# Kernel tuning notes

Measured on AMD Instinct MI355X. Metric: run time of the kernel, lower is better.

The kernel has to match this reference:

```python
import jax, jax.numpy as jnp
import numpy as np

B, K, T, V, H = 32, 5, 20, 9488, 1024


def setup_inputs() -> dict:
    key = jax.random.key(0)
    k0, k1, k2, k3, k4 = jax.random.split(key, 5)
    logprobs = jax.nn.log_softmax(jax.random.normal(k0, (B * K, V), jnp.float32), -1)
    beam_seq = jax.random.randint(k1, (B, K, T), 0, V)
    beam_seq_logprobs = jax.random.normal(k2, (B, K, T, V), jnp.float32)
    beam_logprobs_sum = jax.random.normal(k3, (B, K), jnp.float32)
    state = jax.random.normal(k4, (2, B * K, H), jnp.float32)
    return {"logprobs": logprobs, "beam_seq": beam_seq,
            "beam_seq_logprobs": beam_seq_logprobs,
            "beam_logprobs_sum": beam_logprobs_sum, "state": state,
            "beam_size": K, "t": T}


def reference(logprobs, beam_seq, beam_seq_logprobs, beam_logprobs_sum, state, beam_size, t):
    # One beam_step of CaptionModel.beam_search.
    batch = beam_logprobs_sum.shape[0]
    vocab = logprobs.shape[-1]
    lp = logprobs.reshape(batch, -1, vocab)                  # [B, K, V]
    cand = beam_logprobs_sum[:, :, None] + lp                # [B, K, V]
    flat = cand.reshape(batch, -1)                           # [B, K*V]
    # torch.sort(desc)[:, :beam_size] == top_k (sorted descending)
    ys, ix = jax.lax.top_k(flat, beam_size)                  # [B, K]
    beam_ix = ix // vocab                                    # source beam  [B, K]
    selected_ix = ix % vocab                                 # chosen word  [B, K]
    brange = jnp.arange(batch)[:, None]
    state_ix = (beam_ix + brange * lp.shape[1]).reshape(-1)  # [B*K]

    if t > 0:
        beam_seq = beam_seq[brange, beam_ix]                             # [B, K, t]
        beam_seq_logprobs = beam_seq_logprobs[brange, beam_ix]           # [B, K, t, V]
    beam_seq = jnp.concatenate([beam_seq, selected_ix[:, :, None].astype(beam_seq.dtype)], -1)

    beam_logprobs_sum = (jnp.take_along_axis(beam_logprobs_sum, beam_ix, 1)
                         + jnp.take_along_axis(lp.reshape(batch, -1), ix, 1))  # [B, K]

    beam_lp = lp[brange, beam_ix]                            # [B, K, V]
    beam_seq_logprobs = jnp.concatenate([beam_seq_logprobs, beam_lp[:, :, None, :]], 2)

    new_state = state[:, state_ix]                           # [layers, B*K, H]
    return beam_seq, beam_seq_logprobs, beam_logprobs_sum, new_state
```

## Files before the change

### kernel.cpp

```cpp
#include <hip/hip_runtime.h>

#define BB 32
#define KK 5
#define TT 20
#define VV 9488
#define HH 1024
#define NSPLIT 16
#define CHUNK (VV / NSPLIT)

#define OFF1 3360
#define OFF2 31883040
#define OFF3 31883200

typedef float f4 __attribute__((ext_vector_type(4)));

__device__ __forceinline__ bool better(float av, int ai, float bv, int bi) {
    return (av > bv) || (av == bv && ai < bi);
}

__device__ __forceinline__ void insert5(float tv[5], int ti[5], float val, int idx) {
#pragma unroll
    for (int j = 4; j >= 1; --j) {
        bool bj  = better(val, idx, tv[j],   ti[j]);
        bool bj1 = better(val, idx, tv[j-1], ti[j-1]);
        float nv = bj ? (bj1 ? tv[j-1] : val) : tv[j];
        int   ni = bj ? (bj1 ? ti[j-1] : idx) : ti[j];
        tv[j] = nv; ti[j] = ni;
    }
    bool b0 = better(val, idx, tv[0], ti[0]);
    ti[0] = b0 ? idx : ti[0];
    tv[0] = b0 ? val : tv[0];
}

__device__ __forceinline__ void merge_sorted5(float av[5], int ai[5],
                                              const float bv[5], const int bi[5]) {
    float ov[5]; int oi[5];
#pragma unroll
    for (int n = 0; n < 5; ++n) {
        float mv = 0.f; int mi = 0;
#pragma unroll
        for (int i = 0; i <= n; ++i) {
            const int j = n - i;
            float cv; int ci;
            if (better(av[i], ai[i], bv[j], bi[j])) { cv = av[i]; ci = ai[i]; }
            else                                    { cv = bv[j]; ci = bi[j]; }
            if (i == 0 || better(mv, mi, cv, ci)) { mv = cv; mi = ci; }
        }
        ov[n] = mv; oi[n] = mi;
    }
#pragma unroll
    for (int n = 0; n < 5; ++n) { av[n] = ov[n]; ai[n] = oi[n]; }
}

template<int MAXST>
__device__ __forceinline__ void wave_merge(float tv[5], int ti[5]) {
#pragma unroll
    for (int st = 1; st <= MAXST; st <<= 1) {
        float bv[5]; int bi[5];
#pragma unroll
        for (int j = 0; j < 5; ++j) {
            bv[j] = __shfl_xor(tv[j], st);
            bi[j] = __shfl_xor(ti[j], st);
        }
        merge_sorted5(tv, ti, bv, bi);
    }
}

__global__ __launch_bounds__(256) void topk_part_kernel(
    const float* __restrict__ logprobs,
    const float* __restrict__ sums,
    float* __restrict__ pv,
    int*   __restrict__ pi)
{
    const int b    = blockIdx.x / NSPLIT;
    const int part = blockIdx.x % NSPLIT;
    const int tid  = threadIdx.x;
    const int v0   = part * CHUNK;

    float tv[5]; int ti[5];
#pragma unroll
    for (int j = 0; j < 5; ++j) { tv[j] = -INFINITY; ti[j] = 0x7FFFFF00 + j; }

#pragma unroll
    for (int k = 0; k < KK; ++k) {
        const float s = sums[b * KK + k];
        const float* lp = logprobs + (size_t)(b * KK + k) * VV;
        for (int v = v0 + tid; v < v0 + CHUNK; v += 256)
            insert5(tv, ti, s + lp[v], k * VV + v);
    }

    wave_merge<32>(tv, ti);

    __shared__ float lv[4][5];
    __shared__ int   li[4][5];
    const int wid = tid >> 6, lane = tid & 63;
    if (lane == 0) {
#pragma unroll
        for (int j = 0; j < 5; ++j) { lv[wid][j] = tv[j]; li[wid][j] = ti[j]; }
    }
    __syncthreads();
    if (tid < 64) {
        if (tid < 4) {
#pragma unroll
            for (int j = 0; j < 5; ++j) { tv[j] = lv[tid][j]; ti[j] = li[tid][j]; }
        } else {
#pragma unroll
            for (int j = 0; j < 5; ++j) { tv[j] = -INFINITY; ti[j] = 0x7FFFFF00 + j; }
        }
        wave_merge<2>(tv, ti);
        if (tid == 0) {
#pragma unroll
            for (int j = 0; j < 5; ++j) {
                pv[(size_t)blockIdx.x * 5 + j] = tv[j];
                pi[(size_t)blockIdx.x * 5 + j] = ti[j];
            }
        }
    }
}

__global__ __launch_bounds__(64) void topk_merge_kernel(
    const float* __restrict__ pv,
    const int*   __restrict__ pi,
    int*   __restrict__ ws_beam,
    int*   __restrict__ ws_sel,
    float* __restrict__ ws_sum)
{
    const int b   = blockIdx.x;
    const int tid = threadIdx.x;

    float tv[5]; int ti[5];
    if (tid < NSPLIT) {
        const size_t base = ((size_t)b * NSPLIT + tid) * 5;
#pragma unroll
        for (int j = 0; j < 5; ++j) { tv[j] = pv[base + j]; ti[j] = pi[base + j]; }
    } else {
#pragma unroll
        for (int j = 0; j < 5; ++j) { tv[j] = -INFINITY; ti[j] = 0x7FFFFF00 + j; }
    }

    wave_merge<8>(tv, ti);

    if (tid == 0) {
#pragma unroll
        for (int j = 0; j < 5; ++j) {
            const int idx  = ti[j];
            const int beam = idx / VV;
            ws_beam[b * KK + j] = beam;
            ws_sel [b * KK + j] = idx - beam * VV;
            ws_sum [b * KK + j] = tv[j];
        }
    }
}

__global__ __launch_bounds__(256) void scatter_kernel(
    const float* __restrict__ logprobs,
    const int*   __restrict__ beam_seq_in,
    const float* __restrict__ bslp_in,
    const float* __restrict__ state_in,
    const int*   __restrict__ ws_beam,
    const int*   __restrict__ ws_sel,
    const float* __restrict__ ws_sum,
    float* __restrict__ out)
{
    const int bid = blockIdx.x;
    const int tid = threadIdx.x;
    const int NROWS = BB * KK * (TT + 1);

    if (bid < NROWS) {
        const int b   = bid / (KK * (TT + 1));
        const int rem = bid % (KK * (TT + 1));
        const int k   = rem / (TT + 1);
        const int t   = rem % (TT + 1);
        const int beam = ws_beam[b * KK + k];
        const float* src = (t < TT)
            ? bslp_in  + ((size_t)((b * KK + beam) * TT + t)) * VV
            : logprobs + (size_t)(b * KK + beam) * VV;
        const f4* s4 = (const f4*)src;
        f4* d4 = (f4*)(out + OFF1 + (size_t)bid * VV);
        for (int i = tid; i < VV / 4; i += 256) d4[i] = s4[i];
    } else if (bid < NROWS + 2 * BB * KK) {
        const int r = bid - NROWS;
        const int s = r / (BB * KK);
        const int i = r % (BB * KK);
        const int b = i / KK;
        const int beam = ws_beam[i];
        const f4* s4 = (const f4*)(state_in + ((size_t)s * (BB * KK) + b * KK + beam) * HH);
        f4* d4 = (f4*)(out + OFF3 + (size_t)r * HH);
        for (int j = tid; j < HH / 4; j += 256) d4[j] = s4[j];
    } else {
        for (int j = tid; j < NROWS; j += 256) {
            const int b   = j / (KK * (TT + 1));
            const int rem = j % (KK * (TT + 1));
            const int k   = rem / (TT + 1);
            const int t   = rem % (TT + 1);
            const int bk  = b * KK + k;
            int val;
            if (t < TT) val = beam_seq_in[(size_t)(b * KK + ws_beam[bk]) * TT + t];
            else        val = ws_sel[bk];
            out[j] = (float)val;
        }
        for (int j = tid; j < BB * KK; j += 256) out[OFF2 + j] = ws_sum[j];
    }
}

extern "C" void kernel_launch(void* const* d_in, const int* in_sizes, int n_in,
                              void* d_out, int out_size, void* d_ws, size_t ws_size,
                              hipStream_t stream) {
    const float* logprobs = (const float*)d_in[0];
    const int*   beam_seq = (const int*)  d_in[1];
    const float* bslp     = (const float*)d_in[2];
    const float* sums     = (const float*)d_in[3];
    const float* state    = (const float*)d_in[4];

    float* pv      = (float*)d_ws;
    int*   pi      = (int*)(pv + BB * NSPLIT * 5);
    int*   ws_beam = pi + BB * NSPLIT * 5;
    int*   ws_sel  = ws_beam + BB * KK;
    float* ws_sum  = (float*)(ws_sel + BB * KK);
    float* out     = (float*)d_out;

    topk_part_kernel<<<BB * NSPLIT, 256, 0, stream>>>(logprobs, sums, pv, pi);
    topk_merge_kernel<<<BB, 64, 0, stream>>>(pv, pi, ws_beam, ws_sel, ws_sum);

    const int nblocks = 3360 + 320 + 1;
    scatter_kernel<<<nblocks, 256, 0, stream>>>(logprobs, beam_seq, bslp, state,
                                                ws_beam, ws_sel, ws_sum, out);
}
```

Before: 65.41 us.

## Fuse top-k partial and merge kernels into one 1024-thread block per batch

Replaces the two-stage top-k (16 partial blocks per batch plus a merge kernel) with a single kernel using one 1024-thread block per batch that scans all beams and does the full wave and shared-memory merge. This removes one kernel launch and the workspace round trip for partial results. In exchange, only 32 blocks run the top-k phase, which lowers parallelism across the GPU. The scatter copy loop is also unrolled by two to keep more loads in flight, and the state copy uses a single load per thread.

```diff
diff --git a/kernel.cpp b/kernel.cpp
--- a/kernel.cpp
+++ b/kernel.cpp
@@ -5,8 +5,6 @@
 #define TT 20
 #define VV 9488
 #define HH 1024
-#define NSPLIT 16
-#define CHUNK (VV / NSPLIT)
 
 #define OFF1 3360
 #define OFF2 31883040
@@ -66,16 +64,15 @@
     }
 }
 
-__global__ __launch_bounds__(256) void topk_part_kernel(
+__global__ __launch_bounds__(1024) void topk_kernel(
     const float* __restrict__ logprobs,
     const float* __restrict__ sums,
-    float* __restrict__ pv,
-    int*   __restrict__ pi)
+    int*   __restrict__ ws_beam,
+    int*   __restrict__ ws_sel,
+    float* __restrict__ ws_sum)
 {
-    const int b    = blockIdx.x / NSPLIT;
-    const int part = blockIdx.x % NSPLIT;
-    const int tid  = threadIdx.x;
-    const int v0   = part * CHUNK;
+    const int b   = blockIdx.x;
+    const int tid = threadIdx.x;
 
     float tv[5]; int ti[5];
 #pragma unroll
@@ -85,14 +82,14 @@
     for (int k = 0; k < KK; ++k) {
         const float s = sums[b * KK + k];
         const float* lp = logprobs + (size_t)(b * KK + k) * VV;
-        for (int v = v0 + tid; v < v0 + CHUNK; v += 256)
+        for (int v = tid; v < VV; v += 1024)
             insert5(tv, ti, s + lp[v], k * VV + v);
     }
 
     wave_merge<32>(tv, ti);
 
-    __shared__ float lv[4][5];
-    __shared__ int   li[4][5];
+    __shared__ float lv[16][5];
+    __shared__ int   li[16][5];
     const int wid = tid >> 6, lane = tid & 63;
     if (lane == 0) {
 #pragma unroll
@@ -100,54 +97,23 @@
     }
     __syncthreads();
     if (tid < 64) {
-        if (tid < 4) {
+        if (tid < 16) {
 #pragma unroll
             for (int j = 0; j < 5; ++j) { tv[j] = lv[tid][j]; ti[j] = li[tid][j]; }
         } else {
 #pragma unroll
             for (int j = 0; j < 5; ++j) { tv[j] = -INFINITY; ti[j] = 0x7FFFFF00 + j; }
         }
-        wave_merge<2>(tv, ti);
+        wave_merge<8>(tv, ti);
         if (tid == 0) {
 #pragma unroll
             for (int j = 0; j < 5; ++j) {
-                pv[(size_t)blockIdx.x * 5 + j] = tv[j];
-                pi[(size_t)blockIdx.x * 5 + j] = ti[j];
+                const int idx  = ti[j];
+                const int beam = idx / VV;
+                ws_beam[b * KK + j] = beam;
+                ws_sel [b * KK + j] = idx - beam * VV;
+                ws_sum [b * KK + j] = tv[j];
             }
-        }
-    }
-}
-
-__global__ __launch_bounds__(64) void topk_merge_kernel(
-    const float* __restrict__ pv,
-    const int*   __restrict__ pi,
-    int*   __restrict__ ws_beam,
-    int*   __restrict__ ws_sel,
-    float* __restrict__ ws_sum)
-{
-    const int b   = blockIdx.x;
-    const int tid = threadIdx.x;
-
-    float tv[5]; int ti[5];
-    if (tid < NSPLIT) {
-        const size_t base = ((size_t)b * NSPLIT + tid) * 5;
-#pragma unroll
-        for (int j = 0; j < 5; ++j) { tv[j] = pv[base + j]; ti[j] = pi[base + j]; }
-    } else {
-#pragma unroll
-        for (int j = 0; j < 5; ++j) { tv[j] = -INFINITY; ti[j] = 0x7FFFFF00 + j; }
-    }
-
-    wave_merge<8>(tv, ti);
-
-    if (tid == 0) {
-#pragma unroll
-        for (int j = 0; j < 5; ++j) {
-            const int idx  = ti[j];
-            const int beam = idx / VV;
-            ws_beam[b * KK + j] = beam;
-            ws_sel [b * KK + j] = idx - beam * VV;
-            ws_sum [b * KK + j] = tv[j];
         }
     }
 }
@@ -165,6 +131,7 @@
     const int bid = blockIdx.x;
     const int tid = threadIdx.x;
     const int NROWS = BB * KK * (TT + 1);
+    const int NF4   = VV / 4;
 
     if (bid < NROWS) {
         const int b   = bid / (KK * (TT + 1));
@@ -177,7 +144,14 @@
             : logprobs + (size_t)(b * KK + beam) * VV;
         const f4* s4 = (const f4*)src;
         f4* d4 = (f4*)(out + OFF1 + (size_t)bid * VV);
-        for (int i = tid; i < VV / 4; i += 256) d4[i] = s4[i];
+        int i = tid;
+        for (; i + 256 < NF4; i += 512) {
+            f4 a = s4[i];
+            f4 c = s4[i + 256];
+            d4[i] = a;
+            d4[i + 256] = c;
+        }
+        if (i < NF4) d4[i] = s4[i];
     } else if (bid < NROWS + 2 * BB * KK) {
         const int r = bid - NROWS;
         const int s = r / (BB * KK);
@@ -186,7 +160,7 @@
         const int beam = ws_beam[i];
         const f4* s4 = (const f4*)(state_in + ((size_t)s * (BB * KK) + b * KK + beam) * HH);
         f4* d4 = (f4*)(out + OFF3 + (size_t)r * HH);
-        for (int j = tid; j < HH / 4; j += 256) d4[j] = s4[j];
+        d4[tid] = s4[tid];
     } else {
         for (int j = tid; j < NROWS; j += 256) {
             const int b   = j / (KK * (TT + 1));
@@ -212,15 +186,12 @@
     const float* sums     = (const float*)d_in[3];
     const float* state    = (const float*)d_in[4];
 
-    float* pv      = (float*)d_ws;
-    int*   pi      = (int*)(pv + BB * NSPLIT * 5);
-    int*   ws_beam = pi + BB * NSPLIT * 5;
+    int*   ws_beam = (int*)d_ws;
     int*   ws_sel  = ws_beam + BB * KK;
     float* ws_sum  = (float*)(ws_sel + BB * KK);
     float* out     = (float*)d_out;
 
-    topk_part_kernel<<<BB * NSPLIT, 256, 0, stream>>>(logprobs, sums, pv, pi);
-    topk_merge_kernel<<<BB, 64, 0, stream>>>(pv, pi, ws_beam, ws_sel, ws_sum);
+    topk_kernel<<<BB, 1024, 0, stream>>>(logprobs, sums, ws_beam, ws_sel, ws_sum);
 
     const int nblocks = 3360 + 320 + 1;
     scatter_kernel<<<nblocks, 256, 0, stream>>>(logprobs, beam_seq, bslp, state,
```

Result: slower. 79.92 us (+22.2%).
